# Optimization experiments

Hardware: AMD Instinct MI355X
Metric: run time of the kernel (lower is better)

The kernel has to match this reference:

```python
import jax, jax.numpy as jnp
import numpy as np

T, D, O, L, R = 8192, 4096, 4096, 8, 16  # tokens, in_dim, out_dim, max_loras, lora_rank


def setup_inputs() -> dict:
    key = jax.random.key(0)
    k0, k1, k2, k3, k4 = jax.random.split(key, 5)
    x = jax.random.normal(k0, (T, D), dtype=jnp.float32)
    weight = jax.random.normal(k1, (O, D), dtype=jnp.float32) * 0.02   # base Linear weight
    lora_a = jax.random.normal(k2, (L, R, D), dtype=jnp.float32) * 0.02  # stacked A (slice dim squeezed)
    lora_b = jax.random.normal(k3, (L, O, R), dtype=jnp.float32) * 0.02  # stacked B
    token_lora_idx = jax.random.randint(k4, (T,), 0, L, dtype=jnp.int32)  # per-token adapter id
    return {"x": x, "weight": weight, "lora_a": lora_a, "lora_b": lora_b,
            "token_lora_idx": token_lora_idx}


def reference(x, weight, lora_a, lora_b, token_lora_idx):
    # base linear (no bias)
    base = jnp.einsum('td,od->to', x, weight)
    # punica add_lora_linear, single slice, scale = 1.0:
    # per-token gather of A/B expressed as a one-hot contraction (small L, rank R)
    onehot = jax.nn.one_hot(token_lora_idx, lora_a.shape[0], dtype=x.dtype)  # [T, L]
    shrink = jnp.einsum('td,lrd->tlr', x, lora_a)          # [T, L, R] (tiny: R=16)
    s = jnp.einsum('tlr,tl->tr', shrink, onehot)           # select this token's adapter
    delta = jnp.einsum('tr,lor,tl->to', s, lora_b, onehot) # expand + scatter-add
    return base + delta
```

## Files before the change

### kernel.cpp

```cpp
#include <hip/hip_runtime.h>
#include <hip/hip_bf16.h>
#include <stdint.h>

#define T_TOK 8192
#define DIM 4096
#define ODIM 4096
#define NL 8
#define RANK 16
#define KAUG 4224

__device__ __forceinline__ uint16_t f2b(float x) {
    uint32_t u = __builtin_bit_cast(uint32_t, x);
    u += 0x7fffu + ((u >> 16) & 1u);
    return (uint16_t)(u >> 16);
}

typedef __attribute__((ext_vector_type(4))) float floatx4;
typedef __attribute__((ext_vector_type(8))) __bf16 bf16x8;

__device__ __forceinline__ void load_lds16(const uint16_t* g, uint16_t* l) {
    __builtin_amdgcn_global_load_lds(
        (const __attribute__((address_space(1))) uint32_t*)g,
        (__attribute__((address_space(3))) uint32_t*)l, 16, 0, 0);
}

__global__ __launch_bounds__(256) void pack_all(const float* __restrict__ x,
                                                const float* __restrict__ W,
                                                const float* __restrict__ la,
                                                const float* __restrict__ lb,
                                                uint16_t* __restrict__ xaug,
                                                uint16_t* __restrict__ waug,
                                                uint16_t* __restrict__ aall) {
    int b = blockIdx.x;
    int tid = threadIdx.x;
    const float* src;
    uint16_t* dst;
    if (b < ODIM)               { src = W  + (size_t)b * DIM;                 dst = waug + (size_t)b * KAUG; }
    else if (b < ODIM + T_TOK)  { int t = b - ODIM;
                                  src = x  + (size_t)t * DIM;                 dst = xaug + (size_t)t * KAUG; }
    else                        { int r = b - ODIM - T_TOK;
                                  src = la + (size_t)r * DIM;                 dst = aall + (size_t)r * DIM; }
#pragma unroll
    for (int k = 0; k < 4; ++k) {
        int i4 = k * 256 + tid;
        float4 v = ((const float4*)src)[i4];
        ushort4 bv;
        bv.x = f2b(v.x); bv.y = f2b(v.y); bv.z = f2b(v.z); bv.w = f2b(v.w);
        *(ushort4*)(dst + (size_t)i4 * 4) = bv;
    }
    if (b < ODIM && tid < NL * RANK) {
        int l = tid >> 4, r = tid & 15;
        dst[DIM + tid] = f2b(lb[((size_t)l * ODIM + b) * RANK + r]);
    }
}

#define SBM 32
__global__ __launch_bounds__(256) void shrink_gemm(const uint16_t* __restrict__ xa,
                                                   const uint16_t* __restrict__ aall,
                                                   const int* __restrict__ idx,
                                                   uint16_t* __restrict__ xaug) {
    __shared__ uint16_t sA[SBM * 64];
    __shared__ uint16_t sB[128 * 64];
    int tid = threadIdx.x, lane = tid & 63, wid = tid >> 6;
    int bm = blockIdx.x;
    int q = lane >> 4, r16 = lane & 15;

    int rS = tid >> 3;
    int kcS = (tid & 7) ^ (rS & 7);
    const uint16_t* gA = xa + (size_t)(bm * SBM + rS) * KAUG + kcS * 8;
    const uint16_t* gB0 = aall + (size_t)(rS) * DIM + kcS * 8;
    const uint16_t* gB1 = aall + (size_t)(32 + rS) * DIM + kcS * 8;
    const uint16_t* gB2 = aall + (size_t)(64 + rS) * DIM + kcS * 8;
    const uint16_t* gB3 = aall + (size_t)(96 + rS) * DIM + kcS * 8;
    uint16_t* lA  = sA + wid * 512;
    uint16_t* lB0 = sB + wid * 512;
    uint16_t* lB1 = sB + 2048 + wid * 512;
    uint16_t* lB2 = sB + 4096 + wid * 512;
    uint16_t* lB3 = sB + 6144 + wid * 512;

    int sw0 = (q ^ (r16 & 7)) * 8;
    int sw1 = ((4 + q) ^ (r16 & 7)) * 8;

    floatx4 acc[2][2];
#pragma unroll
    for (int i = 0; i < 2; ++i)
#pragma unroll
        for (int j = 0; j < 2; ++j) acc[i][j] = (floatx4){0.f, 0.f, 0.f, 0.f};

    for (int k0 = 0; k0 < DIM; k0 += 64) {
        __syncthreads();
        load_lds16(gA + k0, lA);
        load_lds16(gB0 + k0, lB0);
        load_lds16(gB1 + k0, lB1);
        load_lds16(gB2 + k0, lB2);
        load_lds16(gB3 + k0, lB3);
        __syncthreads();
#pragma unroll
        for (int kk = 0; kk < 2; ++kk) {
            int sw = kk ? sw1 : sw0;
            bf16x8 af[2], bv[2];
#pragma unroll
            for (int i = 0; i < 2; ++i)
                af[i] = *(const bf16x8*)(sA + (i * 16 + r16) * 64 + sw);
#pragma unroll
            for (int j = 0; j < 2; ++j)
                bv[j] = *(const bf16x8*)(sB + (wid * 32 + j * 16 + r16) * 64 + sw);
#pragma unroll
            for (int i = 0; i < 2; ++i)
#pragma unroll
                for (int j = 0; j < 2; ++j)
                    acc[i][j] = __builtin_amdgcn_mfma_f32_16x16x32_bf16(af[i], bv[j], acc[i][j], 0, 0, 0);
        }
    }
#pragma unroll
    for (int i = 0; i < 2; ++i) {
#pragma unroll
        for (int j = 0; j < 2; ++j) {
            int p = wid * 32 + j * 16 + r16;
            int lp = p >> 4;
#pragma unroll
            for (int e = 0; e < 4; ++e) {
                int t = bm * SBM + i * 16 + q * 4 + e;
                uint16_t v = (idx[t] == lp) ? f2b(acc[i][j][e]) : (uint16_t)0;
                xaug[(size_t)t * KAUG + DIM + p] = v;
            }
        }
    }
}

#define BM 128
#define BN 128

__global__ __launch_bounds__(256) void gemm_aug(const uint16_t* __restrict__ A,
                                                const uint16_t* __restrict__ B,
                                                float* __restrict__ C) {
    __shared__ uint16_t sA[BM * 64];
    __shared__ uint16_t sB[BN * 64];

    int tid = threadIdx.x, lane = tid & 63, wid = tid >> 6;
    int bn = blockIdx.x, bm = blockIdx.y;
    int wm = (wid & 1) * 64, wn = (wid >> 1) * 64;
    int q = lane >> 4, r16 = lane & 15;

    int rS = tid >> 3;
    int kcS = (tid & 7) ^ (rS & 7);
    const uint16_t* gA[4];
    const uint16_t* gB[4];
    uint16_t* lA[4];
    uint16_t* lB[4];
#pragma unroll
    for (int c = 0; c < 4; ++c) {
        gA[c] = A + (size_t)(bm * BM + c * 32 + rS) * KAUG + kcS * 8;
        gB[c] = B + (size_t)(bn * BN + c * 32 + rS) * KAUG + kcS * 8;
        lA[c] = sA + c * 2048 + wid * 512;
        lB[c] = sB + c * 2048 + wid * 512;
    }

    int sw0 = (q ^ (r16 & 7)) * 8;
    int sw1 = ((4 + q) ^ (r16 & 7)) * 8;

    floatx4 acc[4][4];
#pragma unroll
    for (int i = 0; i < 4; ++i)
#pragma unroll
        for (int j = 0; j < 4; ++j) acc[i][j] = (floatx4){0.f, 0.f, 0.f, 0.f};

    for (int k0 = 0; k0 < KAUG; k0 += 64) {
        __syncthreads();
#pragma unroll
        for (int c = 0; c < 4; ++c) {
            load_lds16(gA[c] + k0, lA[c]);
            load_lds16(gB[c] + k0, lB[c]);
        }
        __syncthreads();
#pragma unroll
        for (int kk = 0; kk < 2; ++kk) {
            int sw = kk ? sw1 : sw0;
            bf16x8 af[4], bv[4];
#pragma unroll
            for (int i = 0; i < 4; ++i)
                af[i] = *(const bf16x8*)(sA + (wm + i * 16 + r16) * 64 + sw);
#pragma unroll
            for (int j = 0; j < 4; ++j)
                bv[j] = *(const bf16x8*)(sB + (wn + j * 16 + r16) * 64 + sw);
#pragma unroll
            for (int i = 0; i < 4; ++i)
#pragma unroll
                for (int j = 0; j < 4; ++j)
                    acc[i][j] = __builtin_amdgcn_mfma_f32_16x16x32_bf16(af[i], bv[j], acc[i][j], 0, 0, 0);
        }
    }

#pragma unroll
    for (int i = 0; i < 4; ++i) {
#pragma unroll
        for (int j = 0; j < 4; ++j) {
            int col = bn * BN + wn + j * 16 + r16;
#pragma unroll
            for (int e = 0; e < 4; ++e) {
                int row = bm * BM + wm + i * 16 + q * 4 + e;
                C[(size_t)row * ODIM + col] = acc[i][j][e];
            }
        }
    }
}

extern "C" void kernel_launch(void* const* d_in, const int* in_sizes, int n_in,
                              void* d_out, int out_size, void* d_ws, size_t ws_size,
                              hipStream_t stream) {
    const float* x  = (const float*)d_in[0];
    const float* W  = (const float*)d_in[1];
    const float* la = (const float*)d_in[2];
    const float* lb = (const float*)d_in[3];
    const int* idx  = (const int*)d_in[4];
    float* out = (float*)d_out;

    uint16_t* xaug = (uint16_t*)d_ws;
    uint16_t* waug = xaug + (size_t)T_TOK * KAUG;
    uint16_t* aall = waug + (size_t)ODIM * KAUG;

    hipLaunchKernelGGL(pack_all, dim3(ODIM + T_TOK + NL * RANK), dim3(256), 0, stream,
                       x, W, la, lb, xaug, waug, aall);
    hipLaunchKernelGGL(shrink_gemm, dim3(T_TOK / SBM), dim3(256), 0, stream,
                       xaug, aall, idx, xaug);
    hipLaunchKernelGGL(gemm_aug, dim3(ODIM / BN, T_TOK / BM), dim3(256), 0, stream,
                       xaug, waug, out);
}
```

Measured before the change: 608.2 us.

## Rewrite main GEMM as 256x256 double-buffered 8-wave pipelined kernel

Replaces the 128x128, 4-wave, single-buffered augmented GEMM with a 256x256 tile, 8-wave kernel. It double-buffers LDS and interleaves the global-to-LDS loads of future K tiles with MFMA quadrants, synchronised by manual vmcnt/lgkmcnt waits and raw barriers. It raises MFMA priority with setprio and remaps block IDs across the XCDs for L2 locality. Each tile reuses more data and the load latency is meant to be hidden, at the cost of 128 KB of LDS, high register pressure and fragile hand scheduling.

```diff
diff --git a/kernel.cpp b/kernel.cpp
--- a/kernel.cpp
+++ b/kernel.cpp
@@ -8,6 +8,7 @@
 #define NL 8
 #define RANK 16
 #define KAUG 4224
+#define NKT (KAUG / 64)
 
 __device__ __forceinline__ uint16_t f2b(float x) {
     uint32_t u = __builtin_bit_cast(uint32_t, x);
@@ -128,81 +129,132 @@
     }
 }
 
-#define BM 128
-#define BN 128
-
-__global__ __launch_bounds__(256) void gemm_aug(const uint16_t* __restrict__ A,
-                                                const uint16_t* __restrict__ B,
-                                                float* __restrict__ C) {
-    __shared__ uint16_t sA[BM * 64];
-    __shared__ uint16_t sB[BN * 64];
-
-    int tid = threadIdx.x, lane = tid & 63, wid = tid >> 6;
-    int bn = blockIdx.x, bm = blockIdx.y;
-    int wm = (wid & 1) * 64, wn = (wid >> 1) * 64;
+#define GBM 256
+#define GBN 256
+
+__global__ __launch_bounds__(512) void gemm_aug8(const uint16_t* __restrict__ A,
+                                                 const uint16_t* __restrict__ B,
+                                                 float* __restrict__ C) {
+    __shared__ uint16_t sA[2][GBM * 64];
+    __shared__ uint16_t sB[2][GBN * 64];
+
+    int tid = threadIdx.x;
+    int lane = tid & 63, wid = tid >> 6;
     int q = lane >> 4, r16 = lane & 15;
+    int wm = (wid >> 2) * 128;
+    int wn = (wid & 3) * 64;
+
+    int cpx = gridDim.x >> 3;
+    int wgid = (blockIdx.x & 7) * cpx + (blockIdx.x >> 3);
+    int bn = wgid & 15;
+    int bm = wgid >> 4;
 
     int rS = tid >> 3;
-    int kcS = (tid & 7) ^ (rS & 7);
-    const uint16_t* gA[4];
-    const uint16_t* gB[4];
-    uint16_t* lA[4];
-    uint16_t* lB[4];
-#pragma unroll
-    for (int c = 0; c < 4; ++c) {
-        gA[c] = A + (size_t)(bm * BM + c * 32 + rS) * KAUG + kcS * 8;
-        gB[c] = B + (size_t)(bn * BN + c * 32 + rS) * KAUG + kcS * 8;
-        lA[c] = sA + c * 2048 + wid * 512;
-        lB[c] = sB + c * 2048 + wid * 512;
-    }
-
-    int sw0 = (q ^ (r16 & 7)) * 8;
-    int sw1 = ((4 + q) ^ (r16 & 7)) * 8;
-
-    floatx4 acc[4][4];
-#pragma unroll
-    for (int i = 0; i < 4; ++i)
+    int cS = (tid & 7) ^ (rS & 7);
+    const uint16_t* gA0 = A + (size_t)(bm * GBM + rS) * KAUG + cS * 8;
+    const uint16_t* gB0 = B + (size_t)(bn * GBN + rS) * KAUG + cS * 8;
+    int ldsOff = wid * 512;
+
+    auto stageA = [&](int bufi, int half, int tk) {
+        const uint16_t* g = gA0 + (size_t)(half * 128) * KAUG + (size_t)tk * 64;
+        uint16_t* l = &sA[bufi][half * 8192 + ldsOff];
+        load_lds16(g, l);
+        load_lds16(g + (size_t)64 * KAUG, l + 4096);
+    };
+    auto stageB = [&](int bufi, int half, int tk) {
+        const uint16_t* g = gB0 + (size_t)(half * 128) * KAUG + (size_t)tk * 64;
+        uint16_t* l = &sB[bufi][half * 8192 + ldsOff];
+        load_lds16(g, l);
+        load_lds16(g + (size_t)64 * KAUG, l + 4096);
+    };
+
+    int swz[2] = { ((0 + q) ^ (r16 & 7)) * 8, ((4 + q) ^ (r16 & 7)) * 8 };
+
+    bf16x8 aH[4][2];
+    bf16x8 bfv[4][2];
+    floatx4 acc[8][4];
+#pragma unroll
+    for (int i = 0; i < 8; ++i)
 #pragma unroll
         for (int j = 0; j < 4; ++j) acc[i][j] = (floatx4){0.f, 0.f, 0.f, 0.f};
 
-    for (int k0 = 0; k0 < KAUG; k0 += 64) {
-        __syncthreads();
-#pragma unroll
-        for (int c = 0; c < 4; ++c) {
-            load_lds16(gA[c] + k0, lA[c]);
-            load_lds16(gB[c] + k0, lB[c]);
+    auto rdA = [&](int b, int mh) {
+#pragma unroll
+        for (int mf = 0; mf < 4; ++mf)
+#pragma unroll
+            for (int kk = 0; kk < 2; ++kk)
+                aH[mf][kk] = *(const bf16x8*)&sA[b][(wm + mh * 64 + mf * 16 + r16) * 64 + swz[kk]];
+    };
+    auto rdB = [&](int b) {
+#pragma unroll
+        for (int nf = 0; nf < 4; ++nf)
+#pragma unroll
+            for (int kk = 0; kk < 2; ++kk)
+                bfv[nf][kk] = *(const bf16x8*)&sB[b][(wn + nf * 16 + r16) * 64 + swz[kk]];
+    };
+    auto mmaQ = [&](int mh, int nh) {
+        __builtin_amdgcn_s_setprio(1);
+#pragma unroll
+        for (int mf = 0; mf < 4; ++mf)
+#pragma unroll
+            for (int nf = 0; nf < 2; ++nf)
+#pragma unroll
+                for (int kk = 0; kk < 2; ++kk)
+                    acc[mh * 4 + mf][nh * 2 + nf] = __builtin_amdgcn_mfma_f32_16x16x32_bf16(
+                        aH[mf][kk], bfv[nh * 2 + nf][kk], acc[mh * 4 + mf][nh * 2 + nf], 0, 0, 0);
+        __builtin_amdgcn_s_setprio(0);
+    };
+
+#define BAR  __builtin_amdgcn_s_barrier()
+#define LGK0 { asm volatile("s_waitcnt lgkmcnt(0)" ::: "memory"); __builtin_amdgcn_sched_barrier(0); }
+#define VM6  asm volatile("s_waitcnt vmcnt(6)" ::: "memory")
+#define VM0  asm volatile("s_waitcnt vmcnt(0)" ::: "memory")
+
+    stageB(0, 0, 0); stageB(0, 1, 0); stageA(0, 0, 0); stageA(0, 1, 0);
+    stageB(1, 0, 1); stageB(1, 1, 1); stageA(1, 0, 1);
+    VM6;
+    BAR;
+
+#pragma unroll 1
+    for (int i = 0; i < NKT / 2; ++i) {
+        int t1 = 2 * i + 1, t2 = 2 * i + 2, t3 = 2 * i + 3;
+        rdB(0); rdA(0, 0);
+        stageA(1, 1, t1);
+        BAR; LGK0; mmaQ(0, 0); BAR;
+        if (t2 < NKT) stageB(0, 0, t2);
+        BAR; mmaQ(0, 1); BAR;
+        rdA(0, 1);
+        if (t2 < NKT) stageB(0, 1, t2);
+        BAR; LGK0; mmaQ(1, 0); BAR;
+        if (t2 < NKT) { stageA(0, 0, t2); VM6; } else { VM0; }
+        BAR; mmaQ(1, 1); BAR;
+        rdB(1); rdA(1, 0);
+        if (t2 < NKT) stageA(0, 1, t2);
+        BAR; LGK0; mmaQ(0, 0); BAR;
+        if (t3 < NKT) stageB(1, 0, t3);
+        BAR; mmaQ(0, 1); BAR;
+        rdA(1, 1);
+        if (t3 < NKT) stageB(1, 1, t3);
+        BAR; LGK0; mmaQ(1, 0); BAR;
+        if (t3 < NKT) { stageA(1, 0, t3); VM6; } else { VM0; }
+        BAR; mmaQ(1, 1); BAR;
+    }
+
+#pragma unroll
+    for (int mf = 0; mf < 8; ++mf) {
+#pragma unroll
+        for (int nf = 0; nf < 4; ++nf) {
+            int col = bn * GBN + wn + nf * 16 + r16;
+            int rowb = bm * GBM + wm + mf * 16 + q * 4;
+#pragma unroll
+            for (int e = 0; e < 4; ++e)
+                C[(size_t)(rowb + e) * ODIM + col] = acc[mf][nf][e];
         }
-        __syncthreads();
-#pragma unroll
-        for (int kk = 0; kk < 2; ++kk) {
-            int sw = kk ? sw1 : sw0;
-            bf16x8 af[4], bv[4];
-#pragma unroll
-            for (int i = 0; i < 4; ++i)
-                af[i] = *(const bf16x8*)(sA + (wm + i * 16 + r16) * 64 + sw);
-#pragma unroll
-            for (int j = 0; j < 4; ++j)
-                bv[j] = *(const bf16x8*)(sB + (wn + j * 16 + r16) * 64 + sw);
-#pragma unroll
-            for (int i = 0; i < 4; ++i)
-#pragma unroll
-                for (int j = 0; j < 4; ++j)
-                    acc[i][j] = __builtin_amdgcn_mfma_f32_16x16x32_bf16(af[i], bv[j], acc[i][j], 0, 0, 0);
-        }
-    }
-
-#pragma unroll
-    for (int i = 0; i < 4; ++i) {
-#pragma unroll
-        for (int j = 0; j < 4; ++j) {
-            int col = bn * BN + wn + j * 16 + r16;
-#pragma unroll
-            for (int e = 0; e < 4; ++e) {
-                int row = bm * BM + wm + i * 16 + q * 4 + e;
-                C[(size_t)row * ODIM + col] = acc[i][j][e];
-            }
-        }
-    }
+    }
+#undef BAR
+#undef LGK0
+#undef VM6
+#undef VM0
 }
 
 extern "C" void kernel_launch(void* const* d_in, const int* in_sizes, int n_in,
@@ -223,6 +275,6 @@
                        x, W, la, lb, xaug, waug, aall);
     hipLaunchKernelGGL(shrink_gemm, dim3(T_TOK / SBM), dim3(256), 0, stream,
                        xaug, aall, idx, xaug);
-    hipLaunchKernelGGL(gemm_aug, dim3(ODIM / BN, T_TOK / BM), dim3(256), 0, stream,
+    hipLaunchKernelGGL(gemm_aug8, dim3((T_TOK / GBM) * (ODIM / GBN)), dim3(512), 0, stream,
                        xaug, waug, out);
 }
```

Result: faster. 551.4 us (-9.3%).
